# Optimization experiments

Hardware: AMD Instinct MI355X
Metric: run time of the kernel (lower is better)

Reference implementation:

```python
import jax, jax.numpy as jnp
import numpy as np

MARGIN = 1.0
B, D, NUM_CLASSES = 8192, 128, 10


def setup_inputs() -> dict:
    key = jax.random.key(0)
    k1, k2 = jax.random.split(key)
    embeddings = jax.random.normal(k1, (B, D), dtype=jnp.float32)
    labels = jax.random.randint(k2, (B,), 0, NUM_CLASSES, dtype=jnp.int64)
    return {"embeddings": embeddings, "labels": labels}


def reference(embeddings, labels):
    # pairwise Euclidean distances d[i, j] = sqrt(sum((e_i - e_j)^2))
    sq = jnp.sum(embeddings * embeddings, axis=-1)               # [B]
    d2 = sq[:, None] + sq[None, :] - 2.0 * (embeddings @ embeddings.T)
    dist = jnp.sqrt(jnp.maximum(d2, 0.0))                        # [B, B]

    same = labels[:, None] == labels[None, :]                    # [B, B] bool
    neg_inf = jnp.float32(-jnp.inf)
    pos_inf = jnp.float32(jnp.inf)

    # hardest positive: max distance among same-class (includes self, dist 0, harmless)
    hardest_pos = jnp.max(jnp.where(same, dist, neg_inf), axis=1)   # [B]
    # hardest negative: min distance among different-class
    hardest_neg = jnp.min(jnp.where(same, pos_inf, dist), axis=1)   # [B]

    per_anchor = jax.nn.relu(hardest_pos - hardest_neg + MARGIN)    # [B]
    # use_gt_than_zero_mean=False -> divide by batch size
    return jnp.sum(per_anchor) / per_anchor.shape[0]
```

## Files before the change

kernel.cpp:

```cpp
#include <hip/hip_runtime.h>
#include <hip/hip_bf16.h>
#include <cstdint>

#define BATCH 8192
#define DIM   128
#define KAUG  160
#define MARGIN 1.0f
#define SEP    8192.0f

typedef __attribute__((ext_vector_type(8))) short short8;
typedef __attribute__((ext_vector_type(4))) float f32x4;

__device__ __forceinline__ void async_copy16(const void* g, void* lds) {
    __builtin_amdgcn_global_load_lds(
        (const __attribute__((address_space(1))) unsigned int*)g,
        (__attribute__((address_space(3))) unsigned int*)lds, 16, 0, 0);
}

__global__ __launch_bounds__(256) void bhtl_prep(
    const float* __restrict__ emb,
    const int* __restrict__ labels,
    __hip_bfloat16* __restrict__ EbfA,
    __hip_bfloat16* __restrict__ EbfB,
    float* __restrict__ sq,
    unsigned* __restrict__ hp2,
    unsigned* __restrict__ hn2)
{
    const int w   = threadIdx.x >> 6;
    const int l   = threadIdx.x & 63;
    const int row = blockIdx.x * 4 + w;
    const float2 e = ((const float2*)(emb + row * DIM))[l];
    __hip_bfloat162 h2;
    h2.x = __float2bfloat16(e.x);
    h2.y = __float2bfloat16(e.y);
    ((__hip_bfloat162*)(EbfA + (size_t)row * KAUG))[l] = h2;
    ((__hip_bfloat162*)(EbfB + (size_t)row * KAUG))[l] = h2;
    if (l < 16) {
        const int lab = labels[row];
        const float a0 = (2 * l     == lab) ? 64.f : 0.f;
        const float a1 = (2 * l + 1 == lab) ? 64.f : 0.f;
        __hip_bfloat162 hA, hB;
        hA.x = __float2bfloat16(a0);  hA.y = __float2bfloat16(a1);
        hB.x = __float2bfloat16(-a0); hB.y = __float2bfloat16(-a1);
        ((__hip_bfloat162*)(EbfA + (size_t)row * KAUG + DIM))[l] = hA;
        ((__hip_bfloat162*)(EbfB + (size_t)row * KAUG + DIM))[l] = hB;
    }
    float s = e.x * e.x + e.y * e.y;
    #pragma unroll
    for (int d = 1; d < 64; d <<= 1) s += __shfl_xor(s, d, 64);
    if (l == 0) {
        sq[row]  = s;
        hp2[row] = 0u;
        hn2[row] = 0x7F800000u;
    }
}

__global__ __launch_bounds__(128) void bhtl_main(
    const __hip_bfloat16* __restrict__ EbfA,
    const __hip_bfloat16* __restrict__ EbfB,
    const float* __restrict__ sq,
    unsigned* __restrict__ hp2,
    unsigned* __restrict__ hn2)
{
    __shared__ __align__(16) unsigned short B_s[2][3][2560];
    __shared__ __align__(16) float sqm[2][512];

    const int tid  = threadIdx.x;
    const int w    = tid >> 6;
    const int lane = tid & 63;
    const int q    = lane >> 4;
    const int ln   = lane & 15;
    const int rt   = blockIdx.x >> 4;
    const int js   = blockIdx.x & 15;
    const int rowbase = rt * 128 + w * 64;
    const int jbase   = js * 512;

    short8 af[4][5];
    #pragma unroll
    for (int m = 0; m < 4; ++m)
        #pragma unroll
        for (int kc = 0; kc < 5; ++kc) {
            af[m][kc] = *(const short8*)(
                EbfA + (size_t)(rowbase + m * 16 + ln) * KAUG + kc * 32 + q * 8);
            asm("" : "+v"(af[m][kc]));
        }

    #pragma unroll
    for (int c = 0; c < 2; ++c)
        async_copy16(sq + jbase + (c * 64 + lane) * 4, &sqm[w][c * 256]);

    asm volatile("s_waitcnt vmcnt(0)" ::: "memory");

    auto stageB = [&](int buf, int ch) {
        const int jb = jbase + ch * 16;
        #pragma unroll
        for (int c = 0; c < 5; ++c) {
            int U   = c * 64 + lane;
            int col = U / 20;
            int u   = U - col * 20;
            int g   = (u < 16) ? (u ^ (col & 7)) : u;
            async_copy16(EbfB + (size_t)(jb + col) * KAUG + g * 8,
                         &B_s[w][buf][c * 512]);
        }
    };

    float mp[4] = {-INFINITY, -INFINITY, -INFINITY, -INFINITY};
    float mn[4] = { INFINITY,  INFINITY,  INFINITY,  INFINITY};

    auto doIter = [&](int ch, int buf, bool doStage, bool last) {
        if (last) asm volatile("s_waitcnt vmcnt(0)" ::: "memory");
        else      asm volatile("s_waitcnt vmcnt(5)" ::: "memory");

        short8 bfr[5];
        #pragma unroll
        for (int kc = 0; kc < 5; ++kc) {
            const int t    = kc * 4 + q;
            const int unit = (kc < 4) ? (t ^ (ln & 7)) : t;
            bfr[kc] = *(const short8*)(&B_s[w][buf][(ln * 20 + unit) * 8]);
        }
        f32x4 sqj = *(const f32x4*)(&sqm[w][ch * 16 + q * 4]);

        if (doStage) stageB(buf == 0 ? 2 : buf - 1, ch + 2);

        f32x4 acc[4];
        const f32x4 zero = {0.f, 0.f, 0.f, 0.f};
        #pragma unroll
        for (int m = 0; m < 4; ++m) acc[m] = zero;
        #pragma unroll
        for (int kc = 0; kc < 5; ++kc)
            #pragma unroll
            for (int m = 0; m < 4; ++m)
                acc[m] = __builtin_amdgcn_mfma_f32_16x16x32_bf16(
                    bfr[kc], af[m][kc], acc[m], 0, 0, 0);

        #pragma unroll
        for (int m = 0; m < 4; ++m)
            #pragma unroll
            for (int r = 0; r < 4; ++r) {
                float val = fmaf(-2.0f, acc[m][r], sqj[r]);
                mp[m] = fmaxf(mp[m], val);
                mn[m] = fminf(mn[m], val);
            }
    };

    stageB(0, 0);
    stageB(1, 1);

    #pragma unroll 1
    for (int base = 0; base < 30; base += 3) {
        doIter(base,     0, true, false);
        doIter(base + 1, 1, true, false);
        doIter(base + 2, 2, base + 2 < 30, false);
    }
    doIter(30, 0, false, false);
    doIter(31, 1, false, true);

    #pragma unroll
    for (int m = 0; m < 4; ++m) {
        float a = mp[m], b = mn[m];
        a = fmaxf(a, __shfl_xor(a, 16, 64));
        a = fmaxf(a, __shfl_xor(a, 32, 64));
        b = fminf(b, __shfl_xor(b, 16, 64));
        b = fminf(b, __shfl_xor(b, 32, 64));
        if (q == 0) {
            const int row = rowbase + m * 16 + ln;
            const float sqi = sq[row];
            atomicMax(&hp2[row], __float_as_uint(fmaxf(sqi + a - SEP, 0.0f)));
            atomicMin(&hn2[row], __float_as_uint(fmaxf(sqi + b, 0.0f)));
        }
    }
}

__global__ __launch_bounds__(1024) void bhtl_final(
    const unsigned* __restrict__ hp2,
    const unsigned* __restrict__ hn2,
    float* __restrict__ out)
{
    __shared__ float red[16];
    float sum = 0.f;
    for (int i = threadIdx.x; i < BATCH; i += 1024) {
        float hp = sqrtf(__uint_as_float(hp2[i]));
        float hn = sqrtf(__uint_as_float(hn2[i]));
        sum += fmaxf(hp - hn + MARGIN, 0.f);
    }
    #pragma unroll
    for (int d = 1; d < 64; d <<= 1) sum += __shfl_xor(sum, d, 64);
    int wv = threadIdx.x >> 6;
    if ((threadIdx.x & 63) == 0) red[wv] = sum;
    __syncthreads();
    if (threadIdx.x < 64) {
        float v = (threadIdx.x < 16) ? red[threadIdx.x] : 0.f;
        #pragma unroll
        for (int d = 1; d < 16; d <<= 1) v += __shfl_xor(v, d, 64);
        if (threadIdx.x == 0) out[0] = v / (float)BATCH;
    }
}

extern "C" void kernel_launch(void* const* d_in, const int* in_sizes, int n_in,
                              void* d_out, int out_size, void* d_ws, size_t ws_size,
                              hipStream_t stream)
{
    const float* emb    = (const float*)d_in[0];
    const int*   labels = (const int*)d_in[1];
    float*       out    = (float*)d_out;

    char* ws = (char*)d_ws;
    __hip_bfloat16* EbfA = (__hip_bfloat16*)ws;
    __hip_bfloat16* EbfB = (__hip_bfloat16*)(ws + 3  * 1024 * 1024);
    float*    sq   = (float*)   (ws + 6 * 1024 * 1024);
    unsigned* hp2  = (unsigned*)(ws + 6 * 1024 * 1024 + 32 * 1024);
    unsigned* hn2  = (unsigned*)(ws + 6 * 1024 * 1024 + 64 * 1024);

    bhtl_prep<<<BATCH / 4, 256, 0, stream>>>(emb, labels, EbfA, EbfB, sq, hp2, hn2);
    bhtl_main<<<1024, 128, 0, stream>>>(EbfA, EbfB, sq, hp2, hn2);
    bhtl_final<<<1, 1024, 0, stream>>>(hp2, hn2, out);
}
```

Baseline: 87.64 us.

## Share B tiles between both waves via a 5-deep LDS ring with barriers

```diff
diff --git a/kernel.cpp b/kernel.cpp
--- a/kernel.cpp
+++ b/kernel.cpp
@@ -62,8 +62,8 @@
     unsigned* __restrict__ hp2,
     unsigned* __restrict__ hn2)
 {
-    __shared__ __align__(16) unsigned short B_s[2][3][2560];
-    __shared__ __align__(16) float sqm[2][512];
+    __shared__ __align__(16) unsigned short B_s[5][2560];
+    __shared__ __align__(16) float sqm[512];
 
     const int tid  = threadIdx.x;
     const int w    = tid >> 6;
@@ -75,22 +75,6 @@
     const int rowbase = rt * 128 + w * 64;
     const int jbase   = js * 512;
 
-    short8 af[4][5];
-    #pragma unroll
-    for (int m = 0; m < 4; ++m)
-        #pragma unroll
-        for (int kc = 0; kc < 5; ++kc) {
-            af[m][kc] = *(const short8*)(
-                EbfA + (size_t)(rowbase + m * 16 + ln) * KAUG + kc * 32 + q * 8);
-            asm("" : "+v"(af[m][kc]));
-        }
-
-    #pragma unroll
-    for (int c = 0; c < 2; ++c)
-        async_copy16(sq + jbase + (c * 64 + lane) * 4, &sqm[w][c * 256]);
-
-    asm volatile("s_waitcnt vmcnt(0)" ::: "memory");
-
     auto stageB = [&](int buf, int ch) {
         const int jb = jbase + ch * 16;
         #pragma unroll
@@ -100,27 +84,53 @@
             int u   = U - col * 20;
             int g   = (u < 16) ? (u ^ (col & 7)) : u;
             async_copy16(EbfB + (size_t)(jb + col) * KAUG + g * 8,
-                         &B_s[w][buf][c * 512]);
+                         &B_s[buf][c * 512]);
         }
     };
+
+    short8 af[4][5];
+    float  sqi[4];
+    #pragma unroll
+    for (int m = 0; m < 4; ++m) {
+        const int row = rowbase + m * 16 + ln;
+        #pragma unroll
+        for (int kc = 0; kc < 5; ++kc) {
+            af[m][kc] = *(const short8*)(EbfA + (size_t)row * KAUG + kc * 32 + q * 8);
+            asm("" : "+v"(af[m][kc]));
+        }
+        sqi[m] = sq[row];
+    }
+
+    if (w == 0) {
+        async_copy16(sq + jbase +       lane * 4, &sqm[0]);
+        async_copy16(sq + jbase + 256 + lane * 4, &sqm[256]);
+    }
+    stageB(w,     w);
+    stageB(w + 2, w + 2);
+    asm volatile("s_waitcnt vmcnt(0)" ::: "memory");
+    asm volatile("s_barrier" ::: "memory");
 
     float mp[4] = {-INFINITY, -INFINITY, -INFINITY, -INFINITY};
     float mn[4] = { INFINITY,  INFINITY,  INFINITY,  INFINITY};
 
-    auto doIter = [&](int ch, int buf, bool doStage, bool last) {
-        if (last) asm volatile("s_waitcnt vmcnt(0)" ::: "memory");
-        else      asm volatile("s_waitcnt vmcnt(5)" ::: "memory");
+    auto doIter = [&](int i, int buf, int par, bool doStage, int stageBuf,
+                      bool finalWait) {
+        if (par == w) {
+            if (finalWait) asm volatile("s_waitcnt vmcnt(0)" ::: "memory");
+            else           asm volatile("s_waitcnt vmcnt(5)" ::: "memory");
+        }
+        asm volatile("s_barrier" ::: "memory");
 
         short8 bfr[5];
         #pragma unroll
         for (int kc = 0; kc < 5; ++kc) {
             const int t    = kc * 4 + q;
             const int unit = (kc < 4) ? (t ^ (ln & 7)) : t;
-            bfr[kc] = *(const short8*)(&B_s[w][buf][(ln * 20 + unit) * 8]);
-        }
-        f32x4 sqj = *(const f32x4*)(&sqm[w][ch * 16 + q * 4]);
-
-        if (doStage) stageB(buf == 0 ? 2 : buf - 1, ch + 2);
+            bfr[kc] = *(const short8*)(&B_s[buf][(ln * 20 + unit) * 8]);
+        }
+        f32x4 sqj = *(const f32x4*)(&sqm[i * 16 + q * 4]);
+
+        if (doStage && par == w) stageB(stageBuf, i + 4);
 
         f32x4 acc[4];
         const f32x4 zero = {0.f, 0.f, 0.f, 0.f};
@@ -143,17 +153,16 @@
             }
     };
 
-    stageB(0, 0);
-    stageB(1, 1);
-
     #pragma unroll 1
-    for (int base = 0; base < 30; base += 3) {
-        doIter(base,     0, true, false);
-        doIter(base + 1, 1, true, false);
-        doIter(base + 2, 2, base + 2 < 30, false);
-    }
-    doIter(30, 0, false, false);
-    doIter(31, 1, false, true);
+    for (int base = 0; base < 30; base += 10) {
+        #pragma unroll
+        for (int k = 0; k < 10; ++k) {
+            const int i = base + k;
+            doIter(i, k % 5, k & 1, i <= 27, (k + 4) % 5, false);
+        }
+    }
+    doIter(30, 0, 0, false, 0, true);
+    doIter(31, 1, 1, false, 0, true);
 
     #pragma unroll
     for (int m = 0; m < 4; ++m) {
@@ -164,9 +173,8 @@
         b = fminf(b, __shfl_xor(b, 32, 64));
         if (q == 0) {
             const int row = rowbase + m * 16 + ln;
-            const float sqi = sq[row];
-            atomicMax(&hp2[row], __float_as_uint(fmaxf(sqi + a - SEP, 0.0f)));
-            atomicMin(&hn2[row], __float_as_uint(fmaxf(sqi + b, 0.0f)));
+            atomicMax(&hp2[row], __float_as_uint(fmaxf(sqi[m] + a - SEP, 0.0f)));
+            atomicMin(&hn2[row], __float_as_uint(fmaxf(sqi[m] + b, 0.0f)));
         }
     }
 }
```

Measured after the change: 95.92 us. 9.5% more time.
